# Kernel tuning notes

Hardware: AMD Instinct MI355X
Metric: run time of the kernel (lower is better)

The kernel has to match this reference:

```python
import jax, jax.numpy as jnp
import numpy as np

WIN = (8, 8)
N_WIN_TOK = WIN[0] * WIN[1]  # 64
DIM = 128
HEADS = 4
HEAD_DIM = DIM // HEADS
HIDDEN = int(DIM * 0.25)
B_ = 16384


def _relative_position_index():
    ch = np.arange(WIN[0])
    cw = np.arange(WIN[1])
    coords = np.stack(np.meshgrid(ch, cw, indexing='ij'))      # (2, Wh, Ww)
    flat = coords.reshape(2, -1)                                # (2, N)
    rel = flat[:, :, None] - flat[:, None, :]                   # (2, N, N)
    rel = rel.transpose(1, 2, 0).astype(np.int32)               # (N, N, 2)
    rel[:, :, 0] += WIN[0] - 1
    rel[:, :, 1] += WIN[1] - 1
    rel[:, :, 0] *= 2 * WIN[1] - 1
    return jnp.asarray(rel.sum(-1), dtype=jnp.int32)            # (N, N)


def setup_inputs() -> dict:
    key = jax.random.key(0)
    ks = jax.random.split(key, 8)
    s_in = 1.0 / np.sqrt(DIM)
    s_h = 1.0 / np.sqrt(HIDDEN)
    return {
        'x': jax.random.normal(ks[0], (B_, N_WIN_TOK, DIM), jnp.float32),
        'rpb_table': 0.02 * jax.random.normal(ks[1], ((2 * WIN[0] - 1) * (2 * WIN[1] - 1), HEADS), jnp.float32),
        'wq': s_in * jax.random.normal(ks[2], (DIM, DIM), jnp.float32),
        'bq': jnp.zeros((DIM,), jnp.float32),
        'wkv': s_in * jax.random.normal(ks[3], (DIM, 2 * DIM), jnp.float32),
        'bkv': jnp.zeros((2 * DIM,), jnp.float32),
        'fc1_w': s_in * jax.random.normal(ks[4], (DIM, HIDDEN), jnp.float32),
        'fc1_b': jnp.zeros((HIDDEN,), jnp.float32),
        'fc2_w': s_h * jax.random.normal(ks[5], (HIDDEN, DIM), jnp.float32),
        'fc2_b': jnp.zeros((DIM,), jnp.float32),
        'rel_idx': _relative_position_index(),
    }


def reference(x, rpb_table, wq, bq, wkv, bkv, fc1_w, fc1_b, fc2_w, fc2_b, rel_idx):
    B, N, C = x.shape
    scale = HEAD_DIM ** -0.5
    # qkv projections (Uformer LinearProjection): q from to_q, k/v from to_kv
    q = (x @ wq + bq).reshape(B, N, HEADS, HEAD_DIM).transpose(0, 2, 1, 3)   # (B,h,N,d)
    kv = (x @ wkv + bkv).reshape(B, N, 2, HEADS, HEAD_DIM)
    k = kv[:, :, 0].transpose(0, 2, 1, 3)                                    # (B,h,N,d)
    v = kv[:, :, 1].transpose(0, 2, 1, 3)
    attn = jnp.einsum('bhnd,bhmd->bhnm', q * scale, k)                       # (B,h,N,N)
    bias = rpb_table[rel_idx]                                                # (N,N,h)
    attn = attn + bias.transpose(2, 0, 1)[None]                              # + (1,h,N,N)
    attn = jax.nn.softmax(attn, axis=-1)
    out = jnp.einsum('bhnm,bhmd->bhnd', attn, v).transpose(0, 2, 1, 3).reshape(B, N, C)
    # Mlp proj: fc1 -> GELU -> fc2
    out = jax.nn.gelu(out @ fc1_w + fc1_b, approximate=False) @ fc2_w + fc2_b
    return out
```

## Files before the change

### kernel.cpp

```cpp
#include <hip/hip_runtime.h>
#include <hip/hip_bf16.h>
#include <math.h>

typedef __bf16 bf16x8 __attribute__((ext_vector_type(8)));
typedef __bf16 bf16x4 __attribute__((ext_vector_type(4)));
typedef float f32x4 __attribute__((ext_vector_type(4)));
typedef short s16x4 __attribute__((ext_vector_type(4)));

static __device__ __forceinline__ f32x4 mfma16(bf16x8 a, bf16x8 b, f32x4 c) {
  return __builtin_amdgcn_mfma_f32_16x16x32_bf16(a, b, c, 0, 0, 0);
}
static __device__ __forceinline__ f32x4 mfma1616(s16x4 a, s16x4 b, f32x4 c) {
  return __builtin_amdgcn_mfma_f32_16x16x16bf16_1k(a, b, c, 0, 0, 0);
}
static __device__ __forceinline__ int pk2(float lo, float hi) {
  union { __bf16 h[2]; int i; } u;
  u.h[0] = (__bf16)lo; u.h[1] = (__bf16)hi;
  return u.i;
}
static __device__ __forceinline__ s16x4 mk4(int lo, int hi) {
  union { int d[2]; s16x4 v; } u; u.d[0] = lo; u.d[1] = hi; return u.v;
}


__global__ void wattn_prep(const float* __restrict__ wq, const float* __restrict__ bq,
                           const float* __restrict__ wkv,
                           const float* __restrict__ f1w, const float* __restrict__ f2w,
                           const float* __restrict__ rpb, const int* __restrict__ rel,
                           char* __restrict__ ws)
{
  const int idx = blockIdx.x * 256 + threadIdx.x;
  const float scale = 0.17677669529663687f;
  unsigned short* ws16 = (unsigned short*)ws;
  float* wsf = (float*)ws;

  if (idx < 2048) {
    const int lane = idx & 63, dt = (idx >> 6) & 7, kt = idx >> 9;
    const int gg = lane >> 4, cc = lane & 15;
    bf16x8 v;
#pragma unroll
    for (int i = 0; i < 8; ++i)
      v[i] = (__bf16)(wq[(kt * 32 + gg * 8 + i) * 128 + dt * 16 + cc] * scale);
    *(bf16x8*)(ws16 + idx * 8) = v;
  } else if (idx < 4096) {
    const int e = idx - 2048;
    const int lane = e & 63, dt = (e >> 6) & 7, kt = e >> 9;
    const int gg = lane >> 4, cc = lane & 15;
    bf16x8 v;
#pragma unroll
    for (int i = 0; i < 8; ++i)
      v[i] = (__bf16)(wkv[(kt * 32 + gg * 8 + i) * 256 + dt * 16 + cc]);
    *(bf16x8*)(ws16 + 16384 + e * 8) = v;
  } else if (idx < 6144) {
    const int e = idx - 4096;
    const int lane = e & 63, dt = (e >> 6) & 7, kt = e >> 9;
    const int gg = lane >> 4, cc = lane & 15;
    bf16x8 v;
#pragma unroll
    for (int i = 0; i < 8; ++i)
      v[i] = (__bf16)(wkv[(kt * 32 + gg * 8 + i) * 256 + 128 + dt * 16 + cc]);
    *(bf16x8*)(ws16 + 32768 + e * 8) = v;
  } else if (idx < 7168) {
    const int e = idx - 6144;
    const int lane = e & 63, ht = (e >> 6) & 1, kd = e >> 7;
    const int gg = lane >> 4, cc = lane & 15;
    bf16x4 v;
#pragma unroll
    for (int j = 0; j < 4; ++j)
      v[j] = (__bf16)(f1w[(kd * 16 + gg * 4 + j) * 32 + ht * 16 + cc]);
    *(bf16x4*)(ws16 + 49152 + kd * 512 + lane * 8 + ht * 4) = v;
  } else if (idx < 8192) {
    const int e = idx - 7168;
    const int lane = e & 63, dt = (e >> 6) & 7, hs = e >> 9;
    const int gg = lane >> 4, cc = lane & 15;
    bf16x4 v;
#pragma unroll
    for (int j = 0; j < 4; ++j)
      v[j] = (__bf16)(f2w[(hs * 16 + gg * 4 + j) * 128 + dt * 16 + cc]);
    *(bf16x4*)(ws16 + 53248 + dt * 512 + lane * 8 + hs * 4) = v;
  } else if (idx < 12288) {
    const int e = idx - 8192;
    const int lane = e & 63, nt = (e >> 6) & 3, mt = (e >> 8) & 3, h = e >> 10;
    const int gg = lane >> 4, cc = lane & 15;
    const int q = nt * 16 + cc;
    f32x4 v;
#pragma unroll
    for (int r = 0; r < 4; ++r) {
      const int key = mt * 16 + gg * 4 + r;
      v[r] = rpb[rel[q * 64 + key] * 4 + h];
    }
    *(f32x4*)(wsf + 28672 + e * 4) = v;
  } else if (idx < 12416) {
    const int d = idx - 12288;
    wsf[45056 + d] = bq[d] * scale;
  }
}

__global__ __launch_bounds__(512, 2) void wattn_main(
    const float* __restrict__ x,
    const float* __restrict__ bkv,
    const float* __restrict__ f1b,
    const float* __restrict__ f2b,
    const char* __restrict__ ws,
    float* __restrict__ out,
    int wpb)
{
  extern __shared__ __align__(16) char smem[];
  const int tid = threadIdx.x;
  const int g2 = tid >> 8;
  const int tg = tid & 255;
  const int w = (tid >> 6) & 3;
  const int l = tid & 63;
  const int g = l >> 4;
  const int c = l & 15;

  {
    const f32x4* src = (const f32x4*)ws;
    f32x4* dst = (f32x4*)smem;
#pragma unroll
    for (int i = 0; i < 14; ++i)
      dst[i * 512 + tid] = src[i * 512 + tid];
  }
  __syncthreads();

  const bf16x8* wqp = (const bf16x8*)(smem);
  const bf16x8* wkp = (const bf16x8*)(smem + 32768);
  const bf16x8* wvp = (const bf16x8*)(smem + 65536);
  const int OB = 114688 + g2 * 16384;

  const float* wsf = (const float*)ws;
  const f32x4* biasg = (const f32x4*)(wsf + 28672);
  const float* bqs = wsf + 45056;

  f32x4 biasr[16];
#pragma unroll
  for (int mt = 0; mt < 4; ++mt)
#pragma unroll
    for (int nt = 0; nt < 4; ++nt)
      biasr[mt * 4 + nt] = biasg[((w * 4 + mt) * 4 + nt) * 64 + l];
  f32x4 bq4[2], bk4[2], f1b4[2];
  float bv2[2], f2bb[8];
#pragma unroll
  for (int dt = 0; dt < 2; ++dt) {
    const int dtg = 2 * w + dt;
    bq4[dt] = *(const f32x4*)(bqs + dtg * 16 + g * 4);
    bk4[dt] = *(const f32x4*)(bkv + dtg * 16 + g * 4);
    bv2[dt] = bkv[128 + dtg * 16 + c];
    f1b4[dt] = *(const f32x4*)(f1b + dt * 16 + g * 4);
  }
#pragma unroll
  for (int dt = 0; dt < 8; ++dt) f2bb[dt] = f2b[dt * 16 + c];

  const size_t b0 = ((size_t)blockIdx.x * 2 + g2) * wpb;

  for (int i = 0; i < wpb; ++i) {
    {
      const float* xg = x + (b0 + i) * 8192;
#pragma unroll
      for (int j = 0; j < 8; ++j) {
        const int idx = j * 256 + tg;
        f32x4 v = *((const f32x4*)xg + idx);
        const int row = idx >> 5;
        const int addr = OB + (((row << 8) + ((idx & 31) << 3)) ^ ((row & 7) << 4));
        bf16x4 p = { (__bf16)v[0], (__bf16)v[1], (__bf16)v[2], (__bf16)v[3] };
        *(bf16x4*)(smem + addr) = p;
      }
    }
    __syncthreads();

    bf16x8 xf[4][4];
#pragma unroll
    for (int tt = 0; tt < 4; ++tt) {
      const int row = tt * 16 + c, sw = (row & 7) << 4;
#pragma unroll
      for (int kt = 0; kt < 4; ++kt)
        xf[tt][kt] = *(const bf16x8*)(smem + OB + (((row << 8) + kt * 64 + (g << 4)) ^ sw));
    }
    __syncthreads();

    int qpA[2][4], qpB[2][4], kpA[2][4], kpB[2][4], vpA[2][4], vpB[2][4];
#pragma unroll
    for (int dt = 0; dt < 2; ++dt) {
      const int dtg = 2 * w + dt;
      f32x4 acc[4];
#pragma unroll
      for (int tt = 0; tt < 4; ++tt) acc[tt] = bq4[dt];
#pragma unroll
      for (int kt = 0; kt < 4; ++kt) {
        const bf16x8 wf = wqp[(kt * 8 + dtg) * 64 + l];
#pragma unroll
        for (int tt = 0; tt < 4; ++tt) acc[tt] = mfma16(wf, xf[tt][kt], acc[tt]);
      }
#pragma unroll
      for (int tt = 0; tt < 4; ++tt) {
        qpA[dt][tt] = pk2(acc[tt][0], acc[tt][1]);
        qpB[dt][tt] = pk2(acc[tt][2], acc[tt][3]);
      }
#pragma unroll
      for (int tt = 0; tt < 4; ++tt) acc[tt] = bk4[dt];
#pragma unroll
      for (int kt = 0; kt < 4; ++kt) {
        const bf16x8 wf = wkp[(kt * 8 + dtg) * 64 + l];
#pragma unroll
        for (int tt = 0; tt < 4; ++tt) acc[tt] = mfma16(wf, xf[tt][kt], acc[tt]);
      }
#pragma unroll
      for (int tt = 0; tt < 4; ++tt) {
        kpA[dt][tt] = pk2(acc[tt][0], acc[tt][1]);
        kpB[dt][tt] = pk2(acc[tt][2], acc[tt][3]);
      }
      const float bv = bv2[dt];
#pragma unroll
      for (int tt = 0; tt < 4; ++tt) acc[tt] = (f32x4){ bv, bv, bv, bv };
#pragma unroll
      for (int kt = 0; kt < 4; ++kt) {
        const bf16x8 wf = wvp[(kt * 8 + dtg) * 64 + l];
#pragma unroll
        for (int tt = 0; tt < 4; ++tt) acc[tt] = mfma16(xf[tt][kt], wf, acc[tt]);
      }
#pragma unroll
      for (int tt = 0; tt < 4; ++tt) {
        vpA[dt][tt] = pk2(acc[tt][0], acc[tt][1]);
        vpB[dt][tt] = pk2(acc[tt][2], acc[tt][3]);
      }
    }

    f32x4 s[4][4];
#pragma unroll
    for (int mt = 0; mt < 4; ++mt)
#pragma unroll
      for (int nt = 0; nt < 4; ++nt) {
        f32x4 acc = mfma1616(mk4(kpA[0][mt], kpB[0][mt]),
                             mk4(qpA[0][nt], qpB[0][nt]), biasr[mt * 4 + nt]);
        s[mt][nt] = mfma1616(mk4(kpA[1][mt], kpB[1][mt]),
                             mk4(qpA[1][nt], qpB[1][nt]), acc);
      }

    float rinv[4];
#pragma unroll
    for (int nt = 0; nt < 4; ++nt) {
      float sum = 0.f;
#pragma unroll
      for (int mt = 0; mt < 4; ++mt)
#pragma unroll
        for (int r = 0; r < 4; ++r) {
          const float e = __expf(s[mt][nt][r]);
          s[mt][nt][r] = e;
          sum += e;
        }
      sum += __shfl_xor(sum, 16, 64);
      sum += __shfl_xor(sum, 32, 64);
      rinv[nt] = 1.0f / sum;
    }
    int ppA[4][4], ppB[4][4];
#pragma unroll
    for (int mt = 0; mt < 4; ++mt)
#pragma unroll
      for (int nt = 0; nt < 4; ++nt) {
        ppA[mt][nt] = pk2(s[mt][nt][0], s[mt][nt][1]);
        ppB[mt][nt] = pk2(s[mt][nt][2], s[mt][nt][3]);
      }

#pragma unroll
    for (int nt = 0; nt < 4; ++nt) {
      const float rv = rinv[nt];
#pragma unroll
      for (int dt2 = 0; dt2 < 2; ++dt2) {
        f32x4 acc = { 0.f, 0.f, 0.f, 0.f };
#pragma unroll
        for (int mt = 0; mt < 4; ++mt)
          acc = mfma1616(mk4(vpA[dt2][mt], vpB[dt2][mt]),
                         mk4(ppA[mt][nt], ppB[mt][nt]), acc);
        union { int ii[2]; double d; } u;
        u.ii[0] = pk2(acc[0] * rv, acc[1] * rv);
        u.ii[1] = pk2(acc[2] * rv, acc[3] * rv);
        *(double*)(smem + OB + (((2 * w + dt2) * 4 + nt) * 64 + l) * 8) = u.d;
      }
    }

    __syncthreads();

    {
      int ob[8][2];
#pragma unroll
      for (int kd = 0; kd < 8; ++kd) {
        union { double d; int ii[2]; } u;
        u.d = *(const double*)(smem + OB + ((kd * 4 + w) * 64 + l) * 8);
        ob[kd][0] = u.ii[0]; ob[kd][1] = u.ii[1];
      }
      f32x4 ah0 = f1b4[0], ah1 = f1b4[1];
#pragma unroll
      for (int kd = 0; kd < 8; ++kd) {
        const int4 f1r = *(const int4*)(smem + 98304 + kd * 1024 + l * 16);
        const s16x4 obf = mk4(ob[kd][0], ob[kd][1]);
        ah0 = mfma1616(mk4(f1r.x, f1r.y), obf, ah0);
        ah1 = mfma1616(mk4(f1r.z, f1r.w), obf, ah1);
      }
      int hpA[2], hpB[2];
#pragma unroll
      for (int ht = 0; ht < 2; ++ht) {
        const f32x4 ah = ht ? ah1 : ah0;
        float gv[4];
#pragma unroll
        for (int r = 0; r < 4; ++r) {
          const float v = ah[r];
          gv[r] = v / (1.0f + __expf(-1.5957691216057308f * v * (1.0f + 0.044715f * v * v)));
        }
        hpA[ht] = pk2(gv[0], gv[1]);
        hpB[ht] = pk2(gv[2], gv[3]);
      }
      const s16x4 hf0 = mk4(hpA[0], hpB[0]);
      const s16x4 hf1 = mk4(hpA[1], hpB[1]);
      float* og = out + (b0 + i) * 8192 + (size_t)(w * 16) * 128;
#pragma unroll
      for (int dt = 0; dt < 8; ++dt) {
        const int4 f2r = *(const int4*)(smem + 106496 + dt * 1024 + l * 16);
        f32x4 ay = { f2bb[dt], f2bb[dt], f2bb[dt], f2bb[dt] };
        ay = mfma1616(hf0, mk4(f2r.x, f2r.y), ay);
        ay = mfma1616(hf1, mk4(f2r.z, f2r.w), ay);
#pragma unroll
        for (int r = 0; r < 4; ++r)
          og[(g * 4 + r) * 128 + dt * 16 + c] = ay[r];
      }
    }

    __syncthreads();
  }
}

extern "C" void kernel_launch(void* const* d_in, const int* in_sizes, int n_in,
                              void* d_out, int out_size, void* d_ws, size_t ws_size,
                              hipStream_t stream) {
  const float* x    = (const float*)d_in[0];
  const float* rpb  = (const float*)d_in[1];
  const float* wq   = (const float*)d_in[2];
  const float* bq   = (const float*)d_in[3];
  const float* wkv  = (const float*)d_in[4];
  const float* bkv  = (const float*)d_in[5];
  const float* f1w  = (const float*)d_in[6];
  const float* f1b  = (const float*)d_in[7];
  const float* f2w  = (const float*)d_in[8];
  const float* f2b  = (const float*)d_in[9];
  const int*   rel  = (const int*)d_in[10];
  float* out = (float*)d_out;
  char* ws = (char*)d_ws;
  if (ws_size < 180736) return;

  const int nWin = in_sizes[0] / 8192;
  const int blocks = 512;
  const int wpb = nWin / (blocks * 2);

  hipFuncSetAttribute((const void*)wattn_main,
                      hipFuncAttributeMaxDynamicSharedMemorySize, 147456);

  wattn_prep<<<49, 256, 0, stream>>>(wq, bq, wkv, f1w, f2w, rpb, rel, ws);
  wattn_main<<<blocks, 512, 147456, stream>>>(x, bkv, f1b, f2b, ws, out, wpb);
}
```

Before: 498.7 us.

## Prefetch next window's input into registers and vectorize output stores

```diff
diff --git a/kernel.cpp b/kernel.cpp
--- a/kernel.cpp
+++ b/kernel.cpp
@@ -138,8 +138,8 @@
 #pragma unroll
     for (int nt = 0; nt < 4; ++nt)
       biasr[mt * 4 + nt] = biasg[((w * 4 + mt) * 4 + nt) * 64 + l];
-  f32x4 bq4[2], bk4[2], f1b4[2];
-  float bv2[2], f2bb[8];
+  f32x4 bq4[2], bk4[2], f1b4[2], f2b4[8];
+  float bv2[2];
 #pragma unroll
   for (int dt = 0; dt < 2; ++dt) {
     const int dtg = 2 * w + dt;
@@ -149,23 +149,30 @@
     f1b4[dt] = *(const f32x4*)(f1b + dt * 16 + g * 4);
   }
 #pragma unroll
-  for (int dt = 0; dt < 8; ++dt) f2bb[dt] = f2b[dt * 16 + c];
+  for (int dt = 0; dt < 8; ++dt)
+    f2b4[dt] = *(const f32x4*)(f2b + dt * 16 + g * 4);
 
   const size_t b0 = ((size_t)blockIdx.x * 2 + g2) * wpb;
 
+  int saddr[8];
+#pragma unroll
+  for (int j = 0; j < 8; ++j) {
+    const int idx = j * 256 + tg;
+    const int row = idx >> 5;
+    saddr[j] = OB + (((row << 8) + ((idx & 31) << 3)) ^ ((row & 7) << 4));
+  }
+
+  {
+    const float* xg = x + b0 * 8192;
+#pragma unroll
+    for (int j = 0; j < 8; ++j) {
+      f32x4 v = *((const f32x4*)xg + (j * 256 + tg));
+      bf16x4 p = { (__bf16)v[0], (__bf16)v[1], (__bf16)v[2], (__bf16)v[3] };
+      *(bf16x4*)(smem + saddr[j]) = p;
+    }
+  }
+
   for (int i = 0; i < wpb; ++i) {
-    {
-      const float* xg = x + (b0 + i) * 8192;
-#pragma unroll
-      for (int j = 0; j < 8; ++j) {
-        const int idx = j * 256 + tg;
-        f32x4 v = *((const f32x4*)xg + idx);
-        const int row = idx >> 5;
-        const int addr = OB + (((row << 8) + ((idx & 31) << 3)) ^ ((row & 7) << 4));
-        bf16x4 p = { (__bf16)v[0], (__bf16)v[1], (__bf16)v[2], (__bf16)v[3] };
-        *(bf16x4*)(smem + addr) = p;
-      }
-    }
     __syncthreads();
 
     bf16x8 xf[4][4];
@@ -177,6 +184,14 @@
         xf[tt][kt] = *(const bf16x8*)(smem + OB + (((row << 8) + kt * 64 + (g << 4)) ^ sw));
     }
     __syncthreads();
+
+    f32x4 px[8];
+    if (i + 1 < wpb) {
+      const float* xg = x + (b0 + i + 1) * 8192;
+#pragma unroll
+      for (int j = 0; j < 8; ++j)
+        px[j] = *((const f32x4*)xg + (j * 256 + tg));
+    }
 
     int qpA[2][4], qpB[2][4], kpA[2][4], kpB[2][4], vpA[2][4], vpB[2][4];
 #pragma unroll
@@ -311,20 +326,27 @@
       }
       const s16x4 hf0 = mk4(hpA[0], hpB[0]);
       const s16x4 hf1 = mk4(hpA[1], hpB[1]);
-      float* og = out + (b0 + i) * 8192 + (size_t)(w * 16) * 128;
+      float* og = out + (b0 + i) * 8192 + (size_t)(w * 16 + c) * 128 + g * 4;
 #pragma unroll
       for (int dt = 0; dt < 8; ++dt) {
         const int4 f2r = *(const int4*)(smem + 106496 + dt * 1024 + l * 16);
-        f32x4 ay = { f2bb[dt], f2bb[dt], f2bb[dt], f2bb[dt] };
-        ay = mfma1616(hf0, mk4(f2r.x, f2r.y), ay);
-        ay = mfma1616(hf1, mk4(f2r.z, f2r.w), ay);
-#pragma unroll
-        for (int r = 0; r < 4; ++r)
-          og[(g * 4 + r) * 128 + dt * 16 + c] = ay[r];
+        f32x4 ay = f2b4[dt];
+        ay = mfma1616(mk4(f2r.x, f2r.y), hf0, ay);
+        ay = mfma1616(mk4(f2r.z, f2r.w), hf1, ay);
+        *(f32x4*)(og + dt * 16) = ay;
       }
     }
 
     __syncthreads();
+
+    if (i + 1 < wpb) {
+#pragma unroll
+      for (int j = 0; j < 8; ++j) {
+        bf16x4 p = { (__bf16)px[j][0], (__bf16)px[j][1],
+                     (__bf16)px[j][2], (__bf16)px[j][3] };
+        *(bf16x4*)(smem + saddr[j]) = p;
+      }
+    }
   }
 }
 
```

Result: no change. 492.7 us (-1.2%).

## Hold QKV weights in registers, shrink LDS, launch more smaller blocks

Applied to the files above, without the earlier changes.

```diff
diff --git a/kernel.cpp b/kernel.cpp
--- a/kernel.cpp
+++ b/kernel.cpp
@@ -96,7 +96,7 @@
   }
 }
 
-__global__ __launch_bounds__(512, 2) void wattn_main(
+__global__ __launch_bounds__(256, 2) void wattn_main(
     const float* __restrict__ x,
     const float* __restrict__ bkv,
     const float* __restrict__ f1b,
@@ -105,41 +105,43 @@
     float* __restrict__ out,
     int wpb)
 {
-  extern __shared__ __align__(16) char smem[];
+  __shared__ __align__(16) char smem[32768];
   const int tid = threadIdx.x;
-  const int g2 = tid >> 8;
-  const int tg = tid & 255;
-  const int w = (tid >> 6) & 3;
+  const int w = tid >> 6;
   const int l = tid & 63;
   const int g = l >> 4;
   const int c = l & 15;
+  const int XB = 16384;
 
   {
-    const f32x4* src = (const f32x4*)ws;
+    const f32x4* src = (const f32x4*)(ws + 98304);
     f32x4* dst = (f32x4*)smem;
 #pragma unroll
-    for (int i = 0; i < 14; ++i)
-      dst[i * 512 + tid] = src[i * 512 + tid];
-  }
-  __syncthreads();
-
-  const bf16x8* wqp = (const bf16x8*)(smem);
-  const bf16x8* wkp = (const bf16x8*)(smem + 32768);
-  const bf16x8* wvp = (const bf16x8*)(smem + 65536);
-  const int OB = 114688 + g2 * 16384;
+    for (int i = 0; i < 4; ++i)
+      dst[i * 256 + tid] = src[i * 256 + tid];
+  }
+
+  const bf16x8* wqg = (const bf16x8*)ws;
+  const bf16x8* wkg = (const bf16x8*)(ws + 32768);
+  const bf16x8* wvg = (const bf16x8*)(ws + 65536);
+  bf16x8 wqf[2][4], wkf[2][4], wvf[2][4];
+#pragma unroll
+  for (int dt = 0; dt < 2; ++dt) {
+    const int dtg = 2 * w + dt;
+#pragma unroll
+    for (int kt = 0; kt < 4; ++kt) {
+      wqf[dt][kt] = wqg[(kt * 8 + dtg) * 64 + l];
+      wkf[dt][kt] = wkg[(kt * 8 + dtg) * 64 + l];
+      wvf[dt][kt] = wvg[(kt * 8 + dtg) * 64 + l];
+    }
+  }
 
   const float* wsf = (const float*)ws;
   const f32x4* biasg = (const f32x4*)(wsf + 28672);
   const float* bqs = wsf + 45056;
 
-  f32x4 biasr[16];
-#pragma unroll
-  for (int mt = 0; mt < 4; ++mt)
-#pragma unroll
-    for (int nt = 0; nt < 4; ++nt)
-      biasr[mt * 4 + nt] = biasg[((w * 4 + mt) * 4 + nt) * 64 + l];
   f32x4 bq4[2], bk4[2], f1b4[2];
-  float bv2[2], f2bb[8];
+  float bv2[2];
 #pragma unroll
   for (int dt = 0; dt < 2; ++dt) {
     const int dtg = 2 * w + dt;
@@ -148,22 +150,23 @@
     bv2[dt] = bkv[128 + dtg * 16 + c];
     f1b4[dt] = *(const f32x4*)(f1b + dt * 16 + g * 4);
   }
-#pragma unroll
-  for (int dt = 0; dt < 8; ++dt) f2bb[dt] = f2b[dt * 16 + c];
-
-  const size_t b0 = ((size_t)blockIdx.x * 2 + g2) * wpb;
+
+  const size_t b0 = (size_t)blockIdx.x * wpb;
+  __syncthreads();
 
   for (int i = 0; i < wpb; ++i) {
     {
       const float* xg = x + (b0 + i) * 8192;
 #pragma unroll
-      for (int j = 0; j < 8; ++j) {
-        const int idx = j * 256 + tg;
-        f32x4 v = *((const f32x4*)xg + idx);
-        const int row = idx >> 5;
-        const int addr = OB + (((row << 8) + ((idx & 31) << 3)) ^ ((row & 7) << 4));
-        bf16x4 p = { (__bf16)v[0], (__bf16)v[1], (__bf16)v[2], (__bf16)v[3] };
-        *(bf16x4*)(smem + addr) = p;
+      for (int jj = 0; jj < 4; ++jj) {
+        const int idx0 = jj * 512 + tid * 2;
+        f32x4 u = *((const f32x4*)xg + idx0);
+        f32x4 v = *((const f32x4*)xg + idx0 + 1);
+        const int row = idx0 >> 5;
+        const int addr = XB + ((((row << 8) + ((idx0 & 31) << 3))) ^ ((row & 7) << 4));
+        bf16x8 p = { (__bf16)u[0], (__bf16)u[1], (__bf16)u[2], (__bf16)u[3],
+                     (__bf16)v[0], (__bf16)v[1], (__bf16)v[2], (__bf16)v[3] };
+        *(bf16x8*)(smem + addr) = p;
       }
     }
     __syncthreads();
@@ -174,23 +177,20 @@
       const int row = tt * 16 + c, sw = (row & 7) << 4;
 #pragma unroll
       for (int kt = 0; kt < 4; ++kt)
-        xf[tt][kt] = *(const bf16x8*)(smem + OB + (((row << 8) + kt * 64 + (g << 4)) ^ sw));
+        xf[tt][kt] = *(const bf16x8*)(smem + XB + (((row << 8) + kt * 64 + (g << 4)) ^ sw));
     }
     __syncthreads();
 
     int qpA[2][4], qpB[2][4], kpA[2][4], kpB[2][4], vpA[2][4], vpB[2][4];
 #pragma unroll
     for (int dt = 0; dt < 2; ++dt) {
-      const int dtg = 2 * w + dt;
       f32x4 acc[4];
 #pragma unroll
       for (int tt = 0; tt < 4; ++tt) acc[tt] = bq4[dt];
 #pragma unroll
-      for (int kt = 0; kt < 4; ++kt) {
-        const bf16x8 wf = wqp[(kt * 8 + dtg) * 64 + l];
-#pragma unroll
-        for (int tt = 0; tt < 4; ++tt) acc[tt] = mfma16(wf, xf[tt][kt], acc[tt]);
-      }
+      for (int kt = 0; kt < 4; ++kt)
+#pragma unroll
+        for (int tt = 0; tt < 4; ++tt) acc[tt] = mfma16(wqf[dt][kt], xf[tt][kt], acc[tt]);
 #pragma unroll
       for (int tt = 0; tt < 4; ++tt) {
         qpA[dt][tt] = pk2(acc[tt][0], acc[tt][1]);
@@ -199,11 +199,9 @@
 #pragma unroll
       for (int tt = 0; tt < 4; ++tt) acc[tt] = bk4[dt];
 #pragma unroll
-      for (int kt = 0; kt < 4; ++kt) {
-        const bf16x8 wf = wkp[(kt * 8 + dtg) * 64 + l];
-#pragma unroll
-        for (int tt = 0; tt < 4; ++tt) acc[tt] = mfma16(wf, xf[tt][kt], acc[tt]);
-      }
+      for (int kt = 0; kt < 4; ++kt)
+#pragma unroll
+        for (int tt = 0; tt < 4; ++tt) acc[tt] = mfma16(wkf[dt][kt], xf[tt][kt], acc[tt]);
 #pragma unroll
       for (int tt = 0; tt < 4; ++tt) {
         kpA[dt][tt] = pk2(acc[tt][0], acc[tt][1]);
@@ -213,11 +211,9 @@
 #pragma unroll
       for (int tt = 0; tt < 4; ++tt) acc[tt] = (f32x4){ bv, bv, bv, bv };
 #pragma unroll
-      for (int kt = 0; kt < 4; ++kt) {
-        const bf16x8 wf = wvp[(kt * 8 + dtg) * 64 + l];
-#pragma unroll
-        for (int tt = 0; tt < 4; ++tt) acc[tt] = mfma16(xf[tt][kt], wf, acc[tt]);
-      }
+      for (int kt = 0; kt < 4; ++kt)
+#pragma unroll
+        for (int tt = 0; tt < 4; ++tt) acc[tt] = mfma16(xf[tt][kt], wvf[dt][kt], acc[tt]);
 #pragma unroll
       for (int tt = 0; tt < 4; ++tt) {
         vpA[dt][tt] = pk2(acc[tt][0], acc[tt][1]);
@@ -231,7 +227,8 @@
 #pragma unroll
       for (int nt = 0; nt < 4; ++nt) {
         f32x4 acc = mfma1616(mk4(kpA[0][mt], kpB[0][mt]),
-                             mk4(qpA[0][nt], qpB[0][nt]), biasr[mt * 4 + nt]);
+                             mk4(qpA[0][nt], qpB[0][nt]),
+                             biasg[((w * 4 + mt) * 4 + nt) * 64 + l]);
         s[mt][nt] = mfma1616(mk4(kpA[1][mt], kpB[1][mt]),
                              mk4(qpA[1][nt], qpB[1][nt]), acc);
       }
@@ -274,10 +271,9 @@
         union { int ii[2]; double d; } u;
         u.ii[0] = pk2(acc[0] * rv, acc[1] * rv);
         u.ii[1] = pk2(acc[2] * rv, acc[3] * rv);
-        *(double*)(smem + OB + (((2 * w + dt2) * 4 + nt) * 64 + l) * 8) = u.d;
-      }
-    }
-
+        *(double*)(smem + XB + (((2 * w + dt2) * 4 + nt) * 64 + l) * 8) = u.d;
+      }
+    }
     __syncthreads();
 
     {
@@ -285,13 +281,13 @@
 #pragma unroll
       for (int kd = 0; kd < 8; ++kd) {
         union { double d; int ii[2]; } u;
-        u.d = *(const double*)(smem + OB + ((kd * 4 + w) * 64 + l) * 8);
+        u.d = *(const double*)(smem + XB + ((kd * 4 + w) * 64 + l) * 8);
         ob[kd][0] = u.ii[0]; ob[kd][1] = u.ii[1];
       }
       f32x4 ah0 = f1b4[0], ah1 = f1b4[1];
 #pragma unroll
       for (int kd = 0; kd < 8; ++kd) {
-        const int4 f1r = *(const int4*)(smem + 98304 + kd * 1024 + l * 16);
+        const int4 f1r = *(const int4*)(smem + kd * 1024 + l * 16);
         const s16x4 obf = mk4(ob[kd][0], ob[kd][1]);
         ah0 = mfma1616(mk4(f1r.x, f1r.y), obf, ah0);
         ah1 = mfma1616(mk4(f1r.z, f1r.w), obf, ah1);
@@ -311,19 +307,16 @@
       }
       const s16x4 hf0 = mk4(hpA[0], hpB[0]);
       const s16x4 hf1 = mk4(hpA[1], hpB[1]);
-      float* og = out + (b0 + i) * 8192 + (size_t)(w * 16) * 128;
+      float* og = out + (b0 + i) * 8192 + (size_t)(w * 16 + c) * 128 + g * 4;
 #pragma unroll
       for (int dt = 0; dt < 8; ++dt) {
-        const int4 f2r = *(const int4*)(smem + 106496 + dt * 1024 + l * 16);
-        f32x4 ay = { f2bb[dt], f2bb[dt], f2bb[dt], f2bb[dt] };
-        ay = mfma1616(hf0, mk4(f2r.x, f2r.y), ay);
-        ay = mfma1616(hf1, mk4(f2r.z, f2r.w), ay);
-#pragma unroll
-        for (int r = 0; r < 4; ++r)
-          og[(g * 4 + r) * 128 + dt * 16 + c] = ay[r];
-      }
-    }
-
+        const int4 f2r = *(const int4*)(smem + 8192 + dt * 1024 + l * 16);
+        f32x4 ay = *(const f32x4*)(f2b + dt * 16 + g * 4);
+        ay = mfma1616(mk4(f2r.x, f2r.y), hf0, ay);
+        ay = mfma1616(mk4(f2r.z, f2r.w), hf1, ay);
+        *(f32x4*)(og + dt * 16) = ay;
+      }
+    }
     __syncthreads();
   }
 }
@@ -347,12 +340,9 @@
   if (ws_size < 180736) return;
 
   const int nWin = in_sizes[0] / 8192;
-  const int blocks = 512;
-  const int wpb = nWin / (blocks * 2);
-
-  hipFuncSetAttribute((const void*)wattn_main,
-                      hipFuncAttributeMaxDynamicSharedMemorySize, 147456);
+  const int blocks = 2048;
+  const int wpb = nWin / blocks;
 
   wattn_prep<<<49, 256, 0, stream>>>(wq, bq, wkv, f1w, f2w, rpb, rel, ws);
-  wattn_main<<<blocks, 512, 147456, stream>>>(x, bkv, f1b, f2b, ws, out, wpb);
-}
+  wattn_main<<<blocks, 256, 0, stream>>>(x, bkv, f1b, f2b, ws, out, wpb);
+}
```

After: 664.9 us. 33.3% more time.
